# Optimization experiments

Hardware: AMD Instinct MI355X
Metric: run time of the kernel (lower is better)

## Reference

```python
import jax, jax.numpy as jnp
import numpy as np

B, S, D = 1, 2048, 1024   # batch, seq, hidden_size
I = 2048                  # intermediate_size (mlp1 emits 2*I, SwiGLU halves)
E = 8                     # num_experts
K = 2                     # experts_per_token
LIMIT = 7.0               # swiglu_limit
ALPHA = 1.702             # gpt-oss swiglu alpha
EPS = 1e-5                # RMSNorm eps


def setup_inputs() -> dict:
    key = jax.random.key(0)
    ks = jax.random.split(key, 4)
    s = 0.02
    return {
        "x": jax.random.normal(ks[0], (B, S, D), jnp.float32),
        "norm_scale": jnp.ones((D,), jnp.float32),
        "gate_w": jax.random.normal(ks[1], (D, E), jnp.float32) * s,
        "gate_b": jnp.zeros((E,), jnp.float32),
        "mlp1_w": jax.random.normal(ks[2], (E, D, 2 * I), jnp.float32) * s,
        "mlp1_b": jnp.zeros((E, 2 * I), jnp.float32),
        "mlp2_w": jax.random.normal(ks[3], (E, I, D), jnp.float32) * s,
        "mlp2_b": jnp.zeros((E, D), jnp.float32),
    }


def _swiglu(h):
    # gpt-oss interleaved SwiGLU with clamp limit
    x_glu = jnp.minimum(h[..., ::2], LIMIT)
    x_lin = jnp.clip(h[..., 1::2], -LIMIT, LIMIT)
    return x_glu * jax.nn.sigmoid(ALPHA * x_glu) * (x_lin + 1.0)


def _moe(t, gate_w, gate_b, mlp1_w, mlp1_b, mlp2_w, mlp2_b):
    T = t.shape[0]
    logits = t @ gate_w + gate_b                 # [T, E]
    top_v, top_i = jax.lax.top_k(logits, K)      # [T, K]
    probs = jax.nn.softmax(top_v, axis=-1)       # softmax over selected experts
    # dense routing-weight matrix, zero for unselected experts
    w = jnp.zeros((T, E), t.dtype).at[jnp.arange(T)[:, None], top_i].set(probs)

    def body(acc, ew):
        w1, b1, w2, b2, we = ew                  # per-expert params + weights [T]
        h = _swiglu(t @ w1 + b1)                 # [T, I]
        y = h @ w2 + b2                          # [T, D]
        return acc + we[:, None] * y, None

    acc0 = jnp.zeros((T, t.shape[1]), t.dtype)
    acc, _ = jax.lax.scan(body, acc0, (mlp1_w, mlp1_b, mlp2_w, mlp2_b, w.T))
    return acc


def reference(x, norm_scale, gate_w, gate_b, mlp1_w, mlp1_b, mlp2_w, mlp2_b):
    Bx, Sx, Dx = x.shape
    ms = jnp.mean(x * x, axis=-1, keepdims=True)
    t = (x * jax.lax.rsqrt(ms + EPS) * norm_scale).reshape(Bx * Sx, Dx)
    y = _moe(t, gate_w, gate_b, mlp1_w, mlp1_b, mlp2_w, mlp2_b)
    return x + y.reshape(Bx, Sx, Dx)
```

## Files before the change

kernel.cpp:

```cpp
#include <hip/hip_runtime.h>

typedef unsigned short u16;
typedef __attribute__((ext_vector_type(4))) unsigned short u16x4;
typedef __attribute__((ext_vector_type(8))) unsigned short u16x8;
typedef __attribute__((ext_vector_type(8))) short bf16x8;
typedef __attribute__((ext_vector_type(4))) float f32x4;

#define DEV static __device__ __forceinline__

DEV float bf2f(u16 b){ union{unsigned u; float f;} c; c.u = ((unsigned)b) << 16; return c.f; }
DEV u16 f2bf(float f){ union{float f; unsigned u;} c; c.f = f; unsigned u = c.u; u += 0x7FFF + ((u >> 16) & 1); return (u16)(u >> 16); }

DEV void gload16(const void* g, void* l){
  __builtin_amdgcn_global_load_lds((const __attribute__((address_space(1))) unsigned int*)g,
                                   (__attribute__((address_space(3))) unsigned int*)l, 16, 0, 0);
}

__global__ __launch_bounds__(256) void k_rms(
    const float* __restrict__ x, const float* __restrict__ nsc,
    const float* __restrict__ gw, const float* __restrict__ gb,
    u16* __restrict__ t, int* __restrict__ topi, float* __restrict__ topp)
{
  const int token = blockIdx.x, tid = threadIdx.x;
  const int wv = tid >> 6, lane = tid & 63;
  const float4 xv = *(const float4*)&x[(size_t)token * 1024 + tid * 4];
  float f[4] = {xv.x, xv.y, xv.z, xv.w};
  float ss = f[0]*f[0] + f[1]*f[1] + f[2]*f[2] + f[3]*f[3];
  #pragma unroll
  for (int o = 32; o > 0; o >>= 1) ss += __shfl_down(ss, o, 64);
  __shared__ float red[4];
  __shared__ float s_rs;
  if (lane == 0) red[wv] = ss;
  __syncthreads();
  if (tid == 0) s_rs = rsqrtf((red[0] + red[1] + red[2] + red[3]) * (1.0f / 1024.0f) + 1e-5f);
  __syncthreads();
  const float rs = s_rs;
  const float4 sv = *(const float4*)&nsc[tid * 4];
  const float sc[4] = {sv.x, sv.y, sv.z, sv.w};
  float tf[4]; u16x4 tv;
  #pragma unroll
  for (int j = 0; j < 4; ++j){ tf[j] = f[j] * rs * sc[j]; tv[j] = f2bf(tf[j]); }
  *(u16x4*)&t[(size_t)token * 1024 + tid * 4] = tv;

  float la[8] = {0,0,0,0,0,0,0,0};
  #pragma unroll
  for (int j = 0; j < 4; ++j){
    const int k = tid * 4 + j;
    const float4 g0 = *(const float4*)&gw[k * 8];
    const float4 g1 = *(const float4*)&gw[k * 8 + 4];
    la[0] += tf[j] * g0.x; la[1] += tf[j] * g0.y; la[2] += tf[j] * g0.z; la[3] += tf[j] * g0.w;
    la[4] += tf[j] * g1.x; la[5] += tf[j] * g1.y; la[6] += tf[j] * g1.z; la[7] += tf[j] * g1.w;
  }
  #pragma unroll
  for (int o = 32; o > 0; o >>= 1)
    #pragma unroll
    for (int e = 0; e < 8; ++e) la[e] += __shfl_down(la[e], o, 64);
  __shared__ float lred[4][8];
  if (lane == 0){
    #pragma unroll
    for (int e = 0; e < 8; ++e) lred[wv][e] = la[e];
  }
  __syncthreads();
  if (tid == 0){
    float lg[8];
    #pragma unroll
    for (int e = 0; e < 8; ++e) lg[e] = lred[0][e] + lred[1][e] + lred[2][e] + lred[3][e] + gb[e];
    int i0 = 0;
    for (int e = 1; e < 8; ++e) if (lg[e] > lg[i0]) i0 = e;
    int i1 = -1;
    for (int e = 0; e < 8; ++e) if (e != i0 && (i1 < 0 || lg[e] > lg[i1])) i1 = e;
    const float d = __expf(lg[i1] - lg[i0]);
    const float p0 = 1.0f / (1.0f + d);
    topi[token * 2] = i0; topi[token * 2 + 1] = i1;
    topp[token * 2] = p0; topp[token * 2 + 1] = d * p0;
  }
}

__global__ __launch_bounds__(256) void k_route(
    const int* __restrict__ topi, const float* __restrict__ topp,
    int* __restrict__ cnt, int* __restrict__ offs, int* __restrict__ tok_of,
    float* __restrict__ wt_of, int* __restrict__ slot_of, int* __restrict__ posg)
{
  __shared__ int c[8];
  __shared__ int o[8];
  const int tid = threadIdx.x;
  if (tid < 8) c[tid] = 0;
  __syncthreads();
  for (int a = tid; a < 4096; a += 256){
    int e = topi[a];
    posg[a] = atomicAdd(&c[e], 1);
  }
  __syncthreads();
  if (tid == 0){
    int run = 0;
    for (int e = 0; e < 8; ++e){ o[e] = run; offs[e] = run; cnt[e] = c[e]; run += c[e]; }
  }
  __syncthreads();
  for (int a = tid; a < 4096; a += 256){
    int e = topi[a];
    int s = o[e] + posg[a];
    tok_of[s] = a >> 1;
    wt_of[s] = topp[a];
    slot_of[a] = s;
  }
}

__global__ __launch_bounds__(256) void k_tr(const float* __restrict__ in, u16* __restrict__ outp, int R, int C)
{
  __shared__ __attribute__((aligned(16))) u16 tile[64][72];
  const size_t base = (size_t)blockIdx.z * (size_t)R * (size_t)C;
  const float* src = in + base;
  u16* dst = outp + base;
  const int r0 = blockIdx.y * 64, c0 = blockIdx.x * 64;
  const int tid = threadIdx.x;
  const int lr = tid >> 4;
  const int lc = (tid & 15) * 4;
  #pragma unroll
  for (int i = 0; i < 4; ++i){
    const float4 v = *(const float4*)&src[(size_t)(r0 + lr + i * 16) * C + c0 + lc];
    u16x4 b; b[0] = f2bf(v.x); b[1] = f2bf(v.y); b[2] = f2bf(v.z); b[3] = f2bf(v.w);
    *(u16x4*)&tile[lr + i * 16][lc] = b;
  }
  __syncthreads();
  const int lr2 = tid >> 3;
  const int lc2 = (tid & 7) * 8;
  #pragma unroll
  for (int i = 0; i < 2; ++i){
    const int cc = lr2 + i * 32;
    u16x8 v;
    #pragma unroll
    for (int j = 0; j < 8; ++j) v[j] = tile[lc2 + j][cc];
    *(u16x8*)&dst[(size_t)(c0 + cc) * R + r0 + lc2] = v;
  }
}

__global__ __launch_bounds__(256) void k_gemm1(
    const u16* __restrict__ t, const u16* __restrict__ w1t, const float* __restrict__ b1,
    const int* __restrict__ cnt, const int* __restrict__ offs, const int* __restrict__ tok_of,
    u16* __restrict__ h)
{
  const int e = blockIdx.z;
  const int count = cnt[e];
  const int m0 = blockIdx.y * 128;
  if (m0 >= count) return;
  const int off = offs[e];
  const int n0 = blockIdx.x * 128;

  __shared__ __attribute__((aligned(16))) u16 As[128 * 64];
  __shared__ __attribute__((aligned(16))) u16 Bs[128 * 64];

  const int tid = threadIdx.x, wv = tid >> 6, lane = tid & 63;
  const int arl = lane >> 3;
  const int axu = (lane & 7) ^ arl;

  const u16* asrc[4]; const u16* bsrc[4];
  u16 *adst[4], *bdst[4];
  #pragma unroll
  for (int i = 0; i < 4; ++i){
    const int rr = i * 32 + wv * 8 + arl;
    int r = m0 + rr; if (r > count - 1) r = count - 1;
    asrc[i] = t + (size_t)tok_of[off + r] * 1024 + axu * 8;
    bsrc[i] = w1t + ((size_t)e * 4096 + n0 + rr) * 1024 + axu * 8;
    adst[i] = &As[(i * 32 + wv * 8) * 64];
    bdst[i] = &Bs[(i * 32 + wv * 8) * 64];
  }

  const int wm = wv & 1, wn = wv >> 1;
  const int fr = lane & 15, q = lane >> 4;

  f32x4 acc[4][4];
  #pragma unroll
  for (int a = 0; a < 4; ++a)
    #pragma unroll
    for (int b = 0; b < 4; ++b) acc[a][b] = (f32x4){0.f, 0.f, 0.f, 0.f};

  for (int k0 = 0; k0 < 1024; k0 += 64){
    #pragma unroll
    for (int i = 0; i < 4; ++i){ gload16(asrc[i], adst[i]); asrc[i] += 64; }
    #pragma unroll
    for (int i = 0; i < 4; ++i){ gload16(bsrc[i], bdst[i]); bsrc[i] += 64; }
    __syncthreads();
    #pragma unroll
    for (int hh = 0; hh < 2; ++hh){
      const int pu = (((hh * 4) + q) ^ (fr & 7)) * 8;
      bf16x8 af[4], bq[4];
      #pragma unroll
      for (int fm = 0; fm < 4; ++fm) af[fm] = *(const bf16x8*)&As[(wm * 64 + fm * 16 + fr) * 64 + pu];
      #pragma unroll
      for (int fn = 0; fn < 4; ++fn) bq[fn] = *(const bf16x8*)&Bs[(wn * 64 + fn * 16 + fr) * 64 + pu];
      #pragma unroll
      for (int fm = 0; fm < 4; ++fm)
        #pragma unroll
        for (int fn = 0; fn < 4; ++fn)
          acc[fm][fn] = __builtin_amdgcn_mfma_f32_16x16x32_bf16(af[fm], bq[fn], acc[fm][fn], 0, 0, 0);
    }
    __syncthreads();
  }

  const int cb = n0 + wn * 64 + fr;
  float b1v[4];
  #pragma unroll
  for (int fn = 0; fn < 4; ++fn) b1v[fn] = b1[e * 4096 + cb + fn * 16];
  const int rq = q * 4;
  const bool ev = ((lane & 1) == 0);
  #pragma unroll
  for (int fm = 0; fm < 4; ++fm)
    #pragma unroll
    for (int fn = 0; fn < 4; ++fn)
      #pragma unroll
      for (int r = 0; r < 4; ++r){
        const float val = acc[fm][fn][r] + b1v[fn];
        const float oth = __shfl_xor(val, 1, 64);
        if (ev){
          const int row = m0 + wm * 64 + fm * 16 + rq + r;
          if (row < count){
            const float g = fminf(val, 7.0f);
            const float l = fminf(fmaxf(oth, -7.0f), 7.0f);
            const float o = g / (1.0f + __expf(-1.702f * g)) * (l + 1.0f);
            h[(size_t)(off + row) * 2048 + ((cb + fn * 16) >> 1)] = f2bf(o);
          }
        }
      }
}

__global__ __launch_bounds__(256) void k_gemm2(
    const u16* __restrict__ h, const u16* __restrict__ w2t, const float* __restrict__ b2,
    const int* __restrict__ cnt, const int* __restrict__ offs, const float* __restrict__ wt_of,
    u16* __restrict__ ys)
{
  const int e = blockIdx.z;
  const int count = cnt[e];
  const int m0 = blockIdx.y * 128;
  if (m0 >= count) return;
  const int off = offs[e];
  const int n0 = blockIdx.x * 64;

  __shared__ __attribute__((aligned(16))) u16 As[128 * 64];
  __shared__ __attribute__((aligned(16))) u16 Bs[64 * 64];

  const int tid = threadIdx.x, wv = tid >> 6, lane = tid & 63;
  const int arl = lane >> 3;
  const int axu = (lane & 7) ^ arl;

  const u16* asrc[4]; const u16* bsrc[2];
  u16 *adst[4], *bdst[2];
  #pragma unroll
  for (int i = 0; i < 4; ++i){
    const int rr = i * 32 + wv * 8 + arl;
    int r = m0 + rr; if (r > count - 1) r = count - 1;
    asrc[i] = h + (size_t)(off + r) * 2048 + axu * 8;
    adst[i] = &As[(i * 32 + wv * 8) * 64];
  }
  #pragma unroll
  for (int i = 0; i < 2; ++i){
    const int rr = i * 32 + wv * 8 + arl;
    bsrc[i] = w2t + ((size_t)e * 1024 + n0 + rr) * 2048 + axu * 8;
    bdst[i] = &Bs[(i * 32 + wv * 8) * 64];
  }

  const int wm = wv & 1, wn = wv >> 1;
  const int fr = lane & 15, q = lane >> 4;

  f32x4 acc[4][2];
  #pragma unroll
  for (int a = 0; a < 4; ++a)
    #pragma unroll
    for (int b = 0; b < 2; ++b) acc[a][b] = (f32x4){0.f, 0.f, 0.f, 0.f};

  for (int k0 = 0; k0 < 2048; k0 += 64){
    #pragma unroll
    for (int i = 0; i < 4; ++i){ gload16(asrc[i], adst[i]); asrc[i] += 64; }
    #pragma unroll
    for (int i = 0; i < 2; ++i){ gload16(bsrc[i], bdst[i]); bsrc[i] += 64; }
    __syncthreads();
    #pragma unroll
    for (int hh = 0; hh < 2; ++hh){
      const int pu = (((hh * 4) + q) ^ (fr & 7)) * 8;
      bf16x8 af[4], bq[2];
      #pragma unroll
      for (int fm = 0; fm < 4; ++fm) af[fm] = *(const bf16x8*)&As[(wm * 64 + fm * 16 + fr) * 64 + pu];
      #pragma unroll
      for (int fn = 0; fn < 2; ++fn) bq[fn] = *(const bf16x8*)&Bs[(wn * 32 + fn * 16 + fr) * 64 + pu];
      #pragma unroll
      for (int fm = 0; fm < 4; ++fm)
        #pragma unroll
        for (int fn = 0; fn < 2; ++fn)
          acc[fm][fn] = __builtin_amdgcn_mfma_f32_16x16x32_bf16(af[fm], bq[fn], acc[fm][fn], 0, 0, 0);
    }
    __syncthreads();
  }

  const int cb = n0 + wn * 32 + fr;
  float b2v[2];
  #pragma unroll
  for (int fn = 0; fn < 2; ++fn) b2v[fn] = b2[e * 1024 + cb + fn * 16];
  const int rq = q * 4;
  #pragma unroll
  for (int fm = 0; fm < 4; ++fm)
    #pragma unroll
    for (int rr = 0; rr < 4; ++rr){
      const int row = m0 + wm * 64 + fm * 16 + rq + rr;
      if (row < count){
        const float wt = wt_of[off + row];
        #pragma unroll
        for (int fn = 0; fn < 2; ++fn){
          const float v = (acc[fm][fn][rr] + b2v[fn]) * wt;
          ys[(size_t)(off + row) * 1024 + cb + fn * 16] = f2bf(v);
        }
      }
    }
}

__global__ __launch_bounds__(256) void k_final(
    const float* __restrict__ x, const u16* __restrict__ ys,
    const int* __restrict__ slot_of, float* __restrict__ out)
{
  const int gid = blockIdx.x * 256 + threadIdx.x;
  const int token = gid >> 8;
  const int c0 = (gid & 255) * 4;
  const int s0 = slot_of[token * 2], s1 = slot_of[token * 2 + 1];
  const float4 xv = *(const float4*)&x[(size_t)token * 1024 + c0];
  const u16x4 y0 = *(const u16x4*)&ys[(size_t)s0 * 1024 + c0];
  const u16x4 y1 = *(const u16x4*)&ys[(size_t)s1 * 1024 + c0];
  float4 o;
  o.x = xv.x + bf2f(y0[0]) + bf2f(y1[0]);
  o.y = xv.y + bf2f(y0[1]) + bf2f(y1[1]);
  o.z = xv.z + bf2f(y0[2]) + bf2f(y1[2]);
  o.w = xv.w + bf2f(y0[3]) + bf2f(y1[3]);
  *(float4*)&out[(size_t)token * 1024 + c0] = o;
}

extern "C" void kernel_launch(void* const* d_in, const int* in_sizes, int n_in,
                              void* d_out, int out_size, void* d_ws, size_t ws_size,
                              hipStream_t stream)
{
  const float* x   = (const float*)d_in[0];
  const float* nsc = (const float*)d_in[1];
  const float* gw  = (const float*)d_in[2];
  const float* gb  = (const float*)d_in[3];
  const float* w1  = (const float*)d_in[4];
  const float* b1  = (const float*)d_in[5];
  const float* w2  = (const float*)d_in[6];
  const float* b2  = (const float*)d_in[7];
  float* out = (float*)d_out;
  char* ws = (char*)d_ws;

  size_t o = 0;
  auto alloc = [&](size_t bytes){ size_t r = o; o = (o + bytes + 255) & ~(size_t)255; return r; };
  const size_t o_t    = alloc((size_t)2048 * 1024 * 2);
  const size_t o_w1t  = alloc((size_t)8 * 4096 * 1024 * 2);
  const size_t o_w2t  = alloc((size_t)8 * 1024 * 2048 * 2);
  const size_t o_h    = alloc((size_t)4096 * 2048 * 2);
  const size_t o_ys   = alloc((size_t)4096 * 1024 * 2);
  const size_t o_topi = alloc(4096 * 4);
  const size_t o_topp = alloc(4096 * 4);
  const size_t o_posg = alloc(4096 * 4);
  const size_t o_tok  = alloc(4096 * 4);
  const size_t o_wt   = alloc(4096 * 4);
  const size_t o_slot = alloc(4096 * 4);
  const size_t o_cnt  = alloc(8 * 4);
  const size_t o_offs = alloc(8 * 4);
  if (ws_size < o) return;

  u16*   t_ws  = (u16*)(ws + o_t);
  u16*   w1t   = (u16*)(ws + o_w1t);
  u16*   w2t   = (u16*)(ws + o_w2t);
  u16*   h_ws  = (u16*)(ws + o_h);
  u16*   ys    = (u16*)(ws + o_ys);
  int*   topi  = (int*)(ws + o_topi);
  float* topp  = (float*)(ws + o_topp);
  int*   posg  = (int*)(ws + o_posg);
  int*   tok   = (int*)(ws + o_tok);
  float* wt    = (float*)(ws + o_wt);
  int*   slot  = (int*)(ws + o_slot);
  int*   cnt   = (int*)(ws + o_cnt);
  int*   offs  = (int*)(ws + o_offs);

  k_rms  <<<2048, 256, 0, stream>>>(x, nsc, gw, gb, t_ws, topi, topp);
  k_route<<<1, 256, 0, stream>>>(topi, topp, cnt, offs, tok, wt, slot, posg);
  k_tr   <<<dim3(64, 16, 8), 256, 0, stream>>>(w1, w1t, 1024, 4096);
  k_tr   <<<dim3(16, 32, 8), 256, 0, stream>>>(w2, w2t, 2048, 1024);
  k_gemm1<<<dim3(32, 16, 8), 256, 0, stream>>>(t_ws, w1t, b1, cnt, offs, tok, h_ws);
  k_gemm2<<<dim3(16, 32, 8), 256, 0, stream>>>(h_ws, w2t, b2, cnt, offs, wt, ys);
  k_final<<<2048, 256, 0, stream>>>(x, ys, slot, out);
}
```

Measured before the change: 411.4 us.

## Fuse fp32 weight transpose and bf16 conversion into the expert GEMM loaders

Drops the two standalone kernels that transposed and converted the expert weights to bf16 in workspace. Each GEMM now reads fp32 weight rows straight from the input, converts them to bf16 in registers and writes them transposed into LDS with a new XOR swizzle that matches the fragment reads. This removes a full read-and-write pass over all expert weights plus two launches. In exchange, each M-tile re-reads fp32 weights, which is twice the bytes, and the B-tile load becomes synchronous register loads instead of async global-to-LDS copies. It also trims the gemm2 grid to 16 M-tiles, enough for the largest possible per-expert count.

Result: faster. 384.2 us (-6.6%).

```diff
diff --git a/kernel.cpp b/kernel.cpp
--- a/kernel.cpp
+++ b/kernel.cpp
@@ -1,4 +1,5 @@
 #include <hip/hip_runtime.h>
+#include <hip/hip_bf16.h>
 
 typedef unsigned short u16;
 typedef __attribute__((ext_vector_type(4))) unsigned short u16x4;
@@ -10,6 +11,8 @@
 
 DEV float bf2f(u16 b){ union{unsigned u; float f;} c; c.u = ((unsigned)b) << 16; return c.f; }
 DEV u16 f2bf(float f){ union{float f; unsigned u;} c; c.f = f; unsigned u = c.u; u += 0x7FFF + ((u >> 16) & 1); return (u16)(u >> 16); }
+DEV u16 f2bfh(float f){ union { __hip_bfloat16 h; u16 u; } c; c.h = __float2bfloat16(f); return c.u; }
+DEV float getc(float4 v, int c){ return c == 0 ? v.x : c == 1 ? v.y : c == 2 ? v.z : v.w; }
 
 DEV void gload16(const void* g, void* l){
   __builtin_amdgcn_global_load_lds((const __attribute__((address_space(1))) unsigned int*)g,
@@ -105,37 +108,8 @@
   }
 }
 
-__global__ __launch_bounds__(256) void k_tr(const float* __restrict__ in, u16* __restrict__ outp, int R, int C)
-{
-  __shared__ __attribute__((aligned(16))) u16 tile[64][72];
-  const size_t base = (size_t)blockIdx.z * (size_t)R * (size_t)C;
-  const float* src = in + base;
-  u16* dst = outp + base;
-  const int r0 = blockIdx.y * 64, c0 = blockIdx.x * 64;
-  const int tid = threadIdx.x;
-  const int lr = tid >> 4;
-  const int lc = (tid & 15) * 4;
-  #pragma unroll
-  for (int i = 0; i < 4; ++i){
-    const float4 v = *(const float4*)&src[(size_t)(r0 + lr + i * 16) * C + c0 + lc];
-    u16x4 b; b[0] = f2bf(v.x); b[1] = f2bf(v.y); b[2] = f2bf(v.z); b[3] = f2bf(v.w);
-    *(u16x4*)&tile[lr + i * 16][lc] = b;
-  }
-  __syncthreads();
-  const int lr2 = tid >> 3;
-  const int lc2 = (tid & 7) * 8;
-  #pragma unroll
-  for (int i = 0; i < 2; ++i){
-    const int cc = lr2 + i * 32;
-    u16x8 v;
-    #pragma unroll
-    for (int j = 0; j < 8; ++j) v[j] = tile[lc2 + j][cc];
-    *(u16x8*)&dst[(size_t)(c0 + cc) * R + r0 + lc2] = v;
-  }
-}
-
 __global__ __launch_bounds__(256) void k_gemm1(
-    const u16* __restrict__ t, const u16* __restrict__ w1t, const float* __restrict__ b1,
+    const u16* __restrict__ t, const float* __restrict__ w1, const float* __restrict__ b1,
     const int* __restrict__ cnt, const int* __restrict__ offs, const int* __restrict__ tok_of,
     u16* __restrict__ h)
 {
@@ -153,17 +127,19 @@
   const int arl = lane >> 3;
   const int axu = (lane & 7) ^ arl;
 
-  const u16* asrc[4]; const u16* bsrc[4];
-  u16 *adst[4], *bdst[4];
+  const u16* asrc[4];
+  u16* adst[4];
   #pragma unroll
   for (int i = 0; i < 4; ++i){
     const int rr = i * 32 + wv * 8 + arl;
     int r = m0 + rr; if (r > count - 1) r = count - 1;
     asrc[i] = t + (size_t)tok_of[off + r] * 1024 + axu * 8;
-    bsrc[i] = w1t + ((size_t)e * 4096 + n0 + rr) * 1024 + axu * 8;
     adst[i] = &As[(i * 32 + wv * 8) * 64];
-    bdst[i] = &Bs[(i * 32 + wv * 8) * 64];
-  }
+  }
+
+  const int tkq = tid >> 5;
+  const int tnb = (tid & 31) * 4;
+  const float* bsrc = w1 + (size_t)e * (1024 * 4096) + (size_t)(tkq * 8) * 4096 + n0 + tnb;
 
   const int wm = wv & 1, wn = wv >> 1;
   const int fr = lane & 15, q = lane >> 4;
@@ -177,17 +153,35 @@
   for (int k0 = 0; k0 < 1024; k0 += 64){
     #pragma unroll
     for (int i = 0; i < 4; ++i){ gload16(asrc[i], adst[i]); asrc[i] += 64; }
-    #pragma unroll
-    for (int i = 0; i < 4; ++i){ gload16(bsrc[i], bdst[i]); bsrc[i] += 64; }
+    const float4 fv0 = *(const float4*)(bsrc);
+    const float4 fv1 = *(const float4*)(bsrc + 4096);
+    const float4 fv2 = *(const float4*)(bsrc + 2 * 4096);
+    const float4 fv3 = *(const float4*)(bsrc + 3 * 4096);
+    const float4 fv4 = *(const float4*)(bsrc + 4 * 4096);
+    const float4 fv5 = *(const float4*)(bsrc + 5 * 4096);
+    const float4 fv6 = *(const float4*)(bsrc + 6 * 4096);
+    const float4 fv7 = *(const float4*)(bsrc + 7 * 4096);
+    bsrc += (size_t)64 * 4096;
+    #pragma unroll
+    for (int c = 0; c < 4; ++c){
+      const int nr = tnb + c;
+      u16x8 wq;
+      wq[0] = f2bfh(getc(fv0, c)); wq[1] = f2bfh(getc(fv1, c));
+      wq[2] = f2bfh(getc(fv2, c)); wq[3] = f2bfh(getc(fv3, c));
+      wq[4] = f2bfh(getc(fv4, c)); wq[5] = f2bfh(getc(fv5, c));
+      wq[6] = f2bfh(getc(fv6, c)); wq[7] = f2bfh(getc(fv7, c));
+      *(u16x8*)((char*)Bs + nr * 128 + ((tkq ^ ((nr >> 1) & 7)) << 4)) = wq;
+    }
     __syncthreads();
     #pragma unroll
     for (int hh = 0; hh < 2; ++hh){
-      const int pu = (((hh * 4) + q) ^ (fr & 7)) * 8;
+      const int puA = (((hh * 4) + q) ^ (fr & 7)) * 8;
+      const int puB = (((hh * 4) + q) ^ ((fr >> 1) & 7)) * 8;
       bf16x8 af[4], bq[4];
       #pragma unroll
-      for (int fm = 0; fm < 4; ++fm) af[fm] = *(const bf16x8*)&As[(wm * 64 + fm * 16 + fr) * 64 + pu];
-      #pragma unroll
-      for (int fn = 0; fn < 4; ++fn) bq[fn] = *(const bf16x8*)&Bs[(wn * 64 + fn * 16 + fr) * 64 + pu];
+      for (int fm = 0; fm < 4; ++fm) af[fm] = *(const bf16x8*)&As[(wm * 64 + fm * 16 + fr) * 64 + puA];
+      #pragma unroll
+      for (int fn = 0; fn < 4; ++fn) bq[fn] = *(const bf16x8*)&Bs[(wn * 64 + fn * 16 + fr) * 64 + puB];
       #pragma unroll
       for (int fm = 0; fm < 4; ++fm)
         #pragma unroll
@@ -224,7 +218,7 @@
 }
 
 __global__ __launch_bounds__(256) void k_gemm2(
-    const u16* __restrict__ h, const u16* __restrict__ w2t, const float* __restrict__ b2,
+    const u16* __restrict__ h, const float* __restrict__ w2, const float* __restrict__ b2,
     const int* __restrict__ cnt, const int* __restrict__ offs, const float* __restrict__ wt_of,
     u16* __restrict__ ys)
 {
@@ -242,8 +236,8 @@
   const int arl = lane >> 3;
   const int axu = (lane & 7) ^ arl;
 
-  const u16* asrc[4]; const u16* bsrc[2];
-  u16 *adst[4], *bdst[2];
+  const u16* asrc[4];
+  u16* adst[4];
   #pragma unroll
   for (int i = 0; i < 4; ++i){
     const int rr = i * 32 + wv * 8 + arl;
@@ -251,12 +245,10 @@
     asrc[i] = h + (size_t)(off + r) * 2048 + axu * 8;
     adst[i] = &As[(i * 32 + wv * 8) * 64];
   }
-  #pragma unroll
-  for (int i = 0; i < 2; ++i){
-    const int rr = i * 32 + wv * 8 + arl;
-    bsrc[i] = w2t + ((size_t)e * 1024 + n0 + rr) * 2048 + axu * 8;
-    bdst[i] = &Bs[(i * 32 + wv * 8) * 64];
-  }
+
+  const int tkq = tid >> 4;
+  const int tnb = (tid & 15) * 4;
+  const float* bsrc = w2 + (size_t)e * (2048 * 1024) + (size_t)(tkq * 4) * 1024 + n0 + tnb;
 
   const int wm = wv & 1, wn = wv >> 1;
   const int fr = lane & 15, q = lane >> 4;
@@ -270,17 +262,29 @@
   for (int k0 = 0; k0 < 2048; k0 += 64){
     #pragma unroll
     for (int i = 0; i < 4; ++i){ gload16(asrc[i], adst[i]); asrc[i] += 64; }
-    #pragma unroll
-    for (int i = 0; i < 2; ++i){ gload16(bsrc[i], bdst[i]); bsrc[i] += 64; }
+    const float4 g0 = *(const float4*)(bsrc);
+    const float4 g1 = *(const float4*)(bsrc + 1024);
+    const float4 g2 = *(const float4*)(bsrc + 2 * 1024);
+    const float4 g3 = *(const float4*)(bsrc + 3 * 1024);
+    bsrc += (size_t)64 * 1024;
+    #pragma unroll
+    for (int c = 0; c < 4; ++c){
+      const int nr = tnb + c;
+      u16x4 wd;
+      wd[0] = f2bfh(getc(g0, c)); wd[1] = f2bfh(getc(g1, c));
+      wd[2] = f2bfh(getc(g2, c)); wd[3] = f2bfh(getc(g3, c));
+      *(u16x4*)((char*)Bs + nr * 128 + (((tkq >> 1) ^ ((nr >> 1) & 7)) << 4) + ((tkq & 1) << 3)) = wd;
+    }
     __syncthreads();
     #pragma unroll
     for (int hh = 0; hh < 2; ++hh){
-      const int pu = (((hh * 4) + q) ^ (fr & 7)) * 8;
+      const int puA = (((hh * 4) + q) ^ (fr & 7)) * 8;
+      const int puB = (((hh * 4) + q) ^ ((fr >> 1) & 7)) * 8;
       bf16x8 af[4], bq[2];
       #pragma unroll
-      for (int fm = 0; fm < 4; ++fm) af[fm] = *(const bf16x8*)&As[(wm * 64 + fm * 16 + fr) * 64 + pu];
-      #pragma unroll
-      for (int fn = 0; fn < 2; ++fn) bq[fn] = *(const bf16x8*)&Bs[(wn * 32 + fn * 16 + fr) * 64 + pu];
+      for (int fm = 0; fm < 4; ++fm) af[fm] = *(const bf16x8*)&As[(wm * 64 + fm * 16 + fr) * 64 + puA];
+      #pragma unroll
+      for (int fn = 0; fn < 2; ++fn) bq[fn] = *(const bf16x8*)&Bs[(wn * 32 + fn * 16 + fr) * 64 + puB];
       #pragma unroll
       for (int fm = 0; fm < 4; ++fm)
         #pragma unroll
@@ -348,8 +352,6 @@
   size_t o = 0;
   auto alloc = [&](size_t bytes){ size_t r = o; o = (o + bytes + 255) & ~(size_t)255; return r; };
   const size_t o_t    = alloc((size_t)2048 * 1024 * 2);
-  const size_t o_w1t  = alloc((size_t)8 * 4096 * 1024 * 2);
-  const size_t o_w2t  = alloc((size_t)8 * 1024 * 2048 * 2);
   const size_t o_h    = alloc((size_t)4096 * 2048 * 2);
   const size_t o_ys   = alloc((size_t)4096 * 1024 * 2);
   const size_t o_topi = alloc(4096 * 4);
@@ -363,8 +365,6 @@
   if (ws_size < o) return;
 
   u16*   t_ws  = (u16*)(ws + o_t);
-  u16*   w1t   = (u16*)(ws + o_w1t);
-  u16*   w2t   = (u16*)(ws + o_w2t);
   u16*   h_ws  = (u16*)(ws + o_h);
   u16*   ys    = (u16*)(ws + o_ys);
   int*   topi  = (int*)(ws + o_topi);
@@ -378,9 +378,7 @@
 
   k_rms  <<<2048, 256, 0, stream>>>(x, nsc, gw, gb, t_ws, topi, topp);
   k_route<<<1, 256, 0, stream>>>(topi, topp, cnt, offs, tok, wt, slot, posg);
-  k_tr   <<<dim3(64, 16, 8), 256, 0, stream>>>(w1, w1t, 1024, 4096);
-  k_tr   <<<dim3(16, 32, 8), 256, 0, stream>>>(w2, w2t, 2048, 1024);
-  k_gemm1<<<dim3(32, 16, 8), 256, 0, stream>>>(t_ws, w1t, b1, cnt, offs, tok, h_ws);
-  k_gemm2<<<dim3(16, 32, 8), 256, 0, stream>>>(h_ws, w2t, b2, cnt, offs, wt, ys);
+  k_gemm1<<<dim3(32, 16, 8), 256, 0, stream>>>(t_ws, w1, b1, cnt, offs, tok, h_ws);
+  k_gemm2<<<dim3(16, 16, 8), 256, 0, stream>>>(h_ws, w2, b2, cnt, offs, wt, ys);
   k_final<<<2048, 256, 0, stream>>>(x, ys, slot, out);
 }
```
